# Optimization experiments

Hardware: AMD Instinct MI355X
Metric: run time of the kernel (lower is better)

## Reference

```python
import jax, jax.numpy as jnp
import numpy as np

B, T, D = 32, 2048, 80
K1 = K2 = 3
S1 = S2 = 2
CB_DIM, CB_SIZE = 512, 1024
MASK_P = 0.1
NOISE_STD = 0.1
INPUT_DIM = D * K1 * K2  # 720


def _win_idx(T_in, k, s):
    Tp = (T_in - k) // s + 1
    return jnp.arange(Tp)[:, None] * s + jnp.arange(k)[None, :]  # (Tp, k)


def _unfold(x, k, s):
    # matches torch x.unfold(1, k, s).view(B, Tp, -1): out[b, t, f*k + j] = x[b, t*s + j, f]
    idx = _win_idx(x.shape[1], k, s)
    w = x[:, idx, :]                 # (B, Tp, k, F)
    w = jnp.swapaxes(w, 2, 3)        # (B, Tp, F, k)
    return w.reshape(w.shape[0], w.shape[1], -1)


def setup_inputs() -> dict:
    key = jax.random.key(0)
    k1, k2, k3, k4, k5 = jax.random.split(key, 5)
    raw_feats = jax.random.normal(k1, (B, T, D), jnp.float32)
    auged_feats = jax.random.normal(k2, (B, T, D), jnp.float32)
    length = jax.random.randint(k3, (B,), T // 2, T + 1)
    xav = (2.0 / (INPUT_DIM + CB_DIM)) ** 0.5  # xavier_normal std
    projector = jax.random.normal(k4, (INPUT_DIM, CB_DIM), jnp.float32) * xav
    codebook = jax.random.normal(k5, (CB_SIZE, CB_DIM), jnp.float32)
    return {"raw_feats": raw_feats, "auged_feats": auged_feats, "length": length,
            "projector": projector, "codebook": codebook}


def reference(raw_feats, auged_feats, length, projector, codebook):
    T1 = (T - K1) // S1 + 1
    T2 = (T1 - K2) // S2 + 1
    idx1 = _win_idx(T, K1, S1)                         # (T1, K1)
    idx2 = _win_idx(T1, K2, S2)                        # (T2, K2)
    frame_windows = idx1[idx2].reshape(T2, K1 * K2)    # (T2, 9) original frame idx per subsampled step
    label_lengths = ((length - K1) // S1 + 1 - K2) // S2 + 1  # (B,)

    # --- label path: two torch-style unfolds -> project -> nearest codebook entry ---
    stacked = _unfold(_unfold(raw_feats, K1, S1), K2, S2)     # (B, T2, 720)
    targets = jnp.matmul(stacked, projector)                  # (B, T2, 512)
    # squared-euclidean expansion; same argmin as ||t - c||
    dist = (jnp.sum(targets * targets, axis=-1, keepdims=True)
            - 2.0 * jnp.einsum('btd,cd->btc', targets, codebook)
            + jnp.sum(codebook * codebook, axis=-1))          # (B, T2, 1024)
    labels = jnp.argmin(dist, axis=-1) + 1                    # labels start from 1; 0 = ignore idx
    valid = jnp.arange(T2)[None, :] < label_lengths[:, None]  # (B, T2)
    labels = jnp.where(valid, labels, 0)[None]                # (num_codebooks=1, B, T2)

    # --- static (span length 1) random masking on valid subsampled steps ---
    mkey = jax.random.key(42)
    km, kn = jax.random.split(mkey)
    masked = (jax.random.uniform(km, (B, T2)) < MASK_P) & valid
    masked_dim = masked.astype(jnp.float32)                   # (B, T2)
    # scatter masked subsampled steps back onto original frame indices (union of windows)
    hits = jnp.zeros((B, T), jnp.float32).at[:, frame_windows].add(masked_dim[:, :, None])
    frame_mask = hits > 0                                     # (B, T)
    noise = NOISE_STD * jax.random.normal(kn, (B, T, D), auged_feats.dtype)
    masked_feats = jnp.where(frame_mask[:, :, None], noise, auged_feats)
    return masked_feats, labels, masked_dim
```

## Files before the change

### kernel.cpp

```cpp
#include <hip/hip_runtime.h>
#include <cstdint>

#define B_    32
#define T_    2048
#define D_    80
#define T2_   511
#define NROW  16352
#define GK    720
#define CBD   512
#define CBS   1024
#define HMASK 8176
#define HN    2621440
#define NP    16384
#define KB    23
#define GLDS  (259*81*4)

using bfrag = __attribute__((ext_vector_type(8))) short;
using f32x4 = __attribute__((ext_vector_type(4))) float;
using s8    = __attribute__((ext_vector_type(8))) short;

__device__ inline ushort f2bf(float f){
  uint32_t u = __float_as_uint(f);
  uint32_t r = (u + 0x7FFFu + ((u >> 16) & 1u)) >> 16;
  return (ushort)r;
}
__device__ inline float bf2f(ushort h){ return __uint_as_float(((uint32_t)h) << 16); }

#define GLL16(gsrc, ldst) __builtin_amdgcn_global_load_lds( \
    (__attribute__((address_space(1))) void*)(gsrc), \
    (__attribute__((address_space(3))) void*)(ldst), 16, 0, 0)

__host__ __device__ inline uint32_t rotl_(uint32_t v, int d){ return (v<<d)|(v>>(32-d)); }

__host__ __device__ inline void tf2x32(uint32_t k0, uint32_t k1, uint32_t& x0, uint32_t& x1){
  uint32_t ks2 = k0 ^ k1 ^ 0x1BD11BDAu;
  x0 += k0; x1 += k1;
  const int r0[4] = {13,15,26,6}, r1[4] = {17,29,16,24};
#pragma unroll
  for (int i=0;i<4;i++){ x0 += x1; x1 = rotl_(x1, r0[i]); x1 ^= x0; }
  x0 += k1; x1 += ks2 + 1u;
#pragma unroll
  for (int i=0;i<4;i++){ x0 += x1; x1 = rotl_(x1, r1[i]); x1 ^= x0; }
  x0 += ks2; x1 += k0 + 2u;
#pragma unroll
  for (int i=0;i<4;i++){ x0 += x1; x1 = rotl_(x1, r0[i]); x1 ^= x0; }
  x0 += k0; x1 += k1 + 3u;
#pragma unroll
  for (int i=0;i<4;i++){ x0 += x1; x1 = rotl_(x1, r1[i]); x1 ^= x0; }
  x0 += k1; x1 += ks2 + 4u;
#pragma unroll
  for (int i=0;i<4;i++){ x0 += x1; x1 = rotl_(x1, r0[i]); x1 ^= x0; }
  x0 += ks2; x1 += k0 + 5u;
}

__device__ inline float erfinv_f(float x){
  float w = -log1pf(-x*x);
  float p;
  if (w < 5.0f){
    w -= 2.5f;
    p = 2.81022636e-08f;
    p = fmaf(p, w, 3.43273939e-07f);
    p = fmaf(p, w, -3.5233877e-06f);
    p = fmaf(p, w, -4.39150654e-06f);
    p = fmaf(p, w, 0.00021858087f);
    p = fmaf(p, w, -0.00125372503f);
    p = fmaf(p, w, -0.00417768164f);
    p = fmaf(p, w, 0.246640727f);
    p = fmaf(p, w, 1.50140941f);
  } else {
    w = sqrtf(w) - 3.0f;
    p = -0.000200214257f;
    p = fmaf(p, w, 0.000100950558f);
    p = fmaf(p, w, 0.00134934322f);
    p = fmaf(p, w, -0.00367342844f);
    p = fmaf(p, w, 0.00573950773f);
    p = fmaf(p, w, -0.0076224613f);
    p = fmaf(p, w, 0.00943887047f);
    p = fmaf(p, w, 1.00167406f);
    p = fmaf(p, w, 2.83297682f);
  }
  return p * x;
}

__device__ inline int label_len(int L){ return (((L - 3) / 2) - 2) / 2 + 1; }

__global__ void cbnorm_k(const float* __restrict__ cb, ushort* __restrict__ W0, ushort* __restrict__ W1){
  int c = blockIdx.x, lane = threadIdx.x;
  double s = 0.0;
  for (int k = lane; k < CBD; k += 64){ float v = cb[c*CBD + k]; s += (double)v * (double)v; }
#pragma unroll
  for (int off = 32; off; off >>= 1) s += __shfl_down(s, off);
  float nf = (float)s;
  nf = __shfl(nf, 0);
  size_t base = ((size_t)(KB-1)*CBS + c)*32;
  int sw = ((c >> 1) & 3) << 3;
  if (lane == 16){
    float h = -0.5f * nf;
    ushort h0 = f2bf(h); ushort h1 = f2bf(h - bf2f(h0));
    W0[base + (16 ^ sw)] = h0; W1[base + (16 ^ sw)] = h1;
  } else if (lane > 16 && lane < 32){
    W0[base + (lane ^ sw)] = 0; W1[base + (lane ^ sw)] = 0;
  }
}

__global__ __launch_bounds__(256) void gather_k(const float* __restrict__ raw,
                                                ushort* __restrict__ S0, ushort* __restrict__ S1){
  extern __shared__ float lraw[];
  int b = blockIdx.x >> 3, ch = blockIdx.x & 7;
  int t20 = ch * 64;
  int nt2 = (T2_ - t20 < 64) ? (T2_ - t20) : 64;
  int r0 = 4 * t20;
  int rows = (T_ - r0 < 259) ? (T_ - r0) : 259;
  int tid = threadIdx.x;
  const float4* gsrc = (const float4*)(raw + ((size_t)b*T_ + r0)*D_);
  int nf4 = rows * 20;
  for (int q = tid; q < nf4; q += 256){
    float4 v = gsrc[q];
    int row = q / 20, c4 = (q - row*20) * 4;
    float* dst = &lraw[row*81 + c4];
    dst[0]=v.x; dst[1]=v.y; dst[2]=v.z; dst[3]=v.w;
  }
  __syncthreads();
  int nl = tid >> 2, g = tid & 3;
  if (nl >= nt2) return;
  int n = b*T2_ + t20 + nl;
  int gs = g ^ ((n >> 1) & 3);
  for (int kb = 0; kb < KB; ++kb){
    s8 o0, o1;
#pragma unroll
    for (int j = 0; j < 8; ++j){
      int k = kb*32 + g*8 + j;
      float v = 0.f;
      if (k < GK){
        int d = k / 9, rem = k - 9*d;
        int k1 = rem / 3, k2 = rem - 3*k1;
        v = lraw[(4*nl + 2*k2 + k1)*81 + d];
      } else if (k == GK) v = 1.f;
      ushort h0 = f2bf(v); ushort h1 = f2bf(v - bf2f(h0));
      o0[j] = (short)h0; o1[j] = (short)h1;
    }
    size_t off = ((size_t)kb*NP + n)*32 + gs*8;
    *(s8*)&S0[off] = o0;
    *(s8*)&S1[off] = o1;
  }
}

__global__ __launch_bounds__(256) void wgemm_k(const float* __restrict__ P, const float* __restrict__ cb,
                                               float* __restrict__ Wp){
  __shared__ float sP[16][68];
  __shared__ float sC[16][68];
  int r0 = blockIdx.y * 64, c0 = blockIdx.x * 64;
  int kz = blockIdx.z;
  int tid = threadIdx.x, tx = tid & 15, ty = tid >> 4;
  float acc[4][4] = {};
  for (int k0 = kz * 128; k0 < kz * 128 + 128; k0 += 16){
    __syncthreads();
    {
      int r = tid >> 2, kq = tid & 3;
      int rr = r0 + r;
      float4 v = {0.f,0.f,0.f,0.f};
      if (rr < GK) v = *(const float4*)&P[rr * CBD + k0 + kq * 4];
      sP[kq*4+0][r] = v.x; sP[kq*4+1][r] = v.y; sP[kq*4+2][r] = v.z; sP[kq*4+3][r] = v.w;
      float4 w = *(const float4*)&cb[(c0 + r) * CBD + k0 + kq * 4];
      sC[kq*4+0][r] = w.x; sC[kq*4+1][r] = w.y; sC[kq*4+2][r] = w.z; sC[kq*4+3][r] = w.w;
    }
    __syncthreads();
#pragma unroll
    for (int kk = 0; kk < 16; ++kk){
      float4 a = *(const float4*)&sP[kk][ty * 4];
      float4 b = *(const float4*)&sC[kk][tx * 4];
      float av[4] = {a.x,a.y,a.z,a.w}, bv[4] = {b.x,b.y,b.z,b.w};
#pragma unroll
      for (int i = 0; i < 4; ++i)
#pragma unroll
        for (int j = 0; j < 4; ++j) acc[i][j] = fmaf(av[i], bv[j], acc[i][j]);
    }
  }
#pragma unroll
  for (int i = 0; i < 4; ++i){
    int r = r0 + ty * 4 + i;
    if (r < GK){
      float4 o; o.x = acc[i][0]; o.y = acc[i][1]; o.z = acc[i][2]; o.w = acc[i][3];
      *(float4*)&Wp[((size_t)kz * GK + r) * CBS + c0 + tx * 4] = o;
    }
  }
}

__global__ void wreduce_k(const float* __restrict__ Wp, ushort* __restrict__ W0, ushort* __restrict__ W1){
  int idx = blockIdx.x * 256 + threadIdx.x;
  int r = idx >> 10, c = idx & (CBS - 1);
  float v = Wp[(size_t)r * CBS + c]
          + Wp[((size_t)GK + r) * CBS + c]
          + Wp[((size_t)2*GK + r) * CBS + c]
          + Wp[((size_t)3*GK + r) * CBS + c];
  ushort h0 = f2bf(v); ushort h1 = f2bf(v - bf2f(h0));
  size_t o = ((size_t)(r >> 5) * CBS + c) * 32 + ((r & 31) ^ (((c >> 1) & 3) << 3));
  W0[o] = h0; W1[o] = h1;
}

__global__ __launch_bounds__(512, 2) void score_k(const ushort* __restrict__ S0, const ushort* __restrict__ S1,
                                                  const ushort* __restrict__ W0, const ushort* __restrict__ W1,
                                                  float* __restrict__ pval, int* __restrict__ pidx){
  extern __shared__ ushort lds[];
  int tid = threadIdx.x;
  int lane = tid & 63, wid = tid >> 6;
  int wm = wid >> 2, wn = wid & 3;
  int g = lane >> 4, lr = lane & 15;
  int gsw = g ^ ((lr >> 1) & 3);

  int id = blockIdx.x;
  int xcd = id & 7, slot = id >> 3;
  int cidx = slot & 3, ridx = (xcd << 3) | (slot >> 2);
  int n0 = ridx * 256, c0 = cidx * 256;

  int p = wid >> 1, h = wid & 1;
  const ushort* src0;
  size_t kstride;
  if      (p == 0){ src0 = S0 + (size_t)n0*32; kstride = (size_t)NP*32; }
  else if (p == 1){ src0 = S1 + (size_t)n0*32; kstride = (size_t)NP*32; }
  else if (p == 2){ src0 = W0 + (size_t)c0*32; kstride = (size_t)CBS*32; }
  else            { src0 = W1 + (size_t)c0*32; kstride = (size_t)CBS*32; }
  src0 += h * 4096;
  int doff = p * 8192 + h * 4096;

  f32x4 acc[8][4] = {};

#pragma unroll
  for (int q = 0; q < 8; ++q) GLL16(src0 + q*512 + lane*8, lds + doff + q*512);

  int abase = (wm*128 + lr)*32 + gsw*8;
  int bbase = (wn*64  + lr)*32 + gsw*8;

  for (int kb = 0; kb < KB; ++kb){
    const ushort* cur = lds + (kb & 1) * 32768;
    ushort*       nxt = lds + ((kb & 1) ^ 1) * 32768;
    asm volatile("s_waitcnt vmcnt(0)" ::: "memory");
    __builtin_amdgcn_s_barrier();

    const ushort* A0 = cur;
    const ushort* A1 = cur + 8192;
    const ushort* B0 = cur + 16384;
    const ushort* B1 = cur + 24576;

    bfrag a[4], b0f[4], b1f[4];
#pragma unroll
    for (int mt = 0; mt < 4; ++mt) a[mt] = *(const bfrag*)&A0[abase + mt*512];
#pragma unroll
    for (int nt = 0; nt < 4; ++nt) b0f[nt] = *(const bfrag*)&B0[bbase + nt*512];
    if (kb + 1 < KB){
      const ushort* s = src0 + (size_t)(kb+1)*kstride;
#pragma unroll
      for (int q = 0; q < 8; ++q) GLL16(s + q*512 + lane*8, nxt + doff + q*512);
    }
    asm volatile("s_waitcnt lgkmcnt(0)" ::: "memory");
    __builtin_amdgcn_sched_barrier(0);
    __builtin_amdgcn_s_setprio(1);
#pragma unroll
    for (int mt = 0; mt < 4; ++mt)
#pragma unroll
      for (int nt = 0; nt < 4; ++nt)
        acc[mt][nt] = __builtin_amdgcn_mfma_f32_16x16x32_bf16(a[mt], b0f[nt], acc[mt][nt], 0,0,0);
    __builtin_amdgcn_s_setprio(0);
    __builtin_amdgcn_sched_barrier(0);
    __builtin_amdgcn_s_barrier();
#pragma unroll
    for (int nt = 0; nt < 4; ++nt) b1f[nt] = *(const bfrag*)&B1[bbase + nt*512];
    asm volatile("s_waitcnt lgkmcnt(0)" ::: "memory");
    __builtin_amdgcn_sched_barrier(0);
    __builtin_amdgcn_s_setprio(1);
#pragma unroll
    for (int mt = 0; mt < 4; ++mt)
#pragma unroll
      for (int nt = 0; nt < 4; ++nt)
        acc[mt][nt] = __builtin_amdgcn_mfma_f32_16x16x32_bf16(a[mt], b1f[nt], acc[mt][nt], 0,0,0);
    __builtin_amdgcn_s_setprio(0);
    __builtin_amdgcn_sched_barrier(0);
    __builtin_amdgcn_s_barrier();
#pragma unroll
    for (int mt = 0; mt < 4; ++mt) a[mt] = *(const bfrag*)&A0[abase + (mt+4)*512];
    asm volatile("s_waitcnt lgkmcnt(0)" ::: "memory");
    __builtin_amdgcn_sched_barrier(0);
    __builtin_amdgcn_s_setprio(1);
#pragma unroll
    for (int mt = 0; mt < 4; ++mt)
#pragma unroll
      for (int nt = 0; nt < 4; ++nt)
        acc[4+mt][nt] = __builtin_amdgcn_mfma_f32_16x16x32_bf16(a[mt], b0f[nt], acc[4+mt][nt], 0,0,0);
#pragma unroll
    for (int mt = 0; mt < 4; ++mt)
#pragma unroll
      for (int nt = 0; nt < 4; ++nt)
        acc[4+mt][nt] = __builtin_amdgcn_mfma_f32_16x16x32_bf16(a[mt], b1f[nt], acc[4+mt][nt], 0,0,0);
    __builtin_amdgcn_s_setprio(0);
    __builtin_amdgcn_sched_barrier(0);
    __builtin_amdgcn_s_barrier();
    bfrag a1f[8];
#pragma unroll
    for (int mt = 0; mt < 8; ++mt) a1f[mt] = *(const bfrag*)&A1[abase + mt*512];
    asm volatile("s_waitcnt lgkmcnt(0)" ::: "memory");
    __builtin_amdgcn_sched_barrier(0);
    __builtin_amdgcn_s_setprio(1);
#pragma unroll
    for (int mt = 0; mt < 8; ++mt)
#pragma unroll
      for (int nt = 0; nt < 4; ++nt)
        acc[mt][nt] = __builtin_amdgcn_mfma_f32_16x16x32_bf16(a1f[mt], b0f[nt], acc[mt][nt], 0,0,0);
    __builtin_amdgcn_s_setprio(0);
    __builtin_amdgcn_sched_barrier(0);
  }

#pragma unroll
  for (int mt = 0; mt < 8; ++mt){
    float bv[4]; int bi[4];
#pragma unroll
    for (int r = 0; r < 4; ++r){
      float best = 3.4e38f; int besti = 0;
#pragma unroll
      for (int nt = 0; nt < 4; ++nt){
        float d = -2.f * acc[mt][nt][r];
        int c = c0 + wn*64 + nt*16 + lr;
        if (d < best){ best = d; besti = c; }
      }
      bv[r] = best; bi[r] = besti;
    }
#pragma unroll
    for (int off = 1; off < 16; off <<= 1){
#pragma unroll
      for (int r = 0; r < 4; ++r){
        float ov = __shfl_xor(bv[r], off);
        int   oi = __shfl_xor(bi[r], off);
        if (ov < bv[r] || (ov == bv[r] && oi < bi[r])){ bv[r] = ov; bi[r] = oi; }
      }
    }
    if (lr == 0){
      int pp = cidx*4 + wn;
#pragma unroll
      for (int r = 0; r < 4; ++r){
        int n = n0 + wm*128 + mt*16 + g*4 + r;
        pval[(size_t)pp*NP + n] = bv[r];
        pidx[(size_t)pp*NP + n] = bi[r];
      }
    }
  }
}

__device__ inline void emit_mask(const int* len, float* md, int i, uint32_t bits){
  float u = __uint_as_float((bits >> 9) | 0x3F800000u) - 1.0f;
  int b = i / T2_, t2 = i - b * T2_;
  bool m = (u < 0.1f) && (t2 < label_len(len[b]));
  md[i] = m ? 1.0f : 0.0f;
}

__device__ inline void comb_one(const float* __restrict__ pval, const int* __restrict__ pidx,
                                const int* __restrict__ len, float* __restrict__ lb, int n){
  float bv = pval[n]; int bi = pidx[n];
#pragma unroll
  for (int p = 1; p < 16; ++p){
    float v = pval[(size_t)p*NP + n]; int ii = pidx[(size_t)p*NP + n];
    if (v < bv || (v == bv && ii < bi)){ bv = v; bi = ii; }
  }
  int b = n / T2_, t2 = n - b * T2_;
  lb[n] = (t2 < label_len(len[b])) ? (float)(bi + 1) : 0.f;
}

__global__ void maskcomb_k(const float* __restrict__ pval, const int* __restrict__ pidx,
                           const int* __restrict__ len, float* __restrict__ lb,
                           float* __restrict__ md, uint32_t km0, uint32_t km1){
  int j = blockIdx.x * 256 + threadIdx.x;
  if (j >= HMASK) return;
  uint32_t x0 = (uint32_t)j, x1 = (uint32_t)(j + HMASK);
  tf2x32(km0, km1, x0, x1);
  emit_mask(len, md, j, x0);
  emit_mask(len, md, j + HMASK, x1);
  comb_one(pval, pidx, len, lb, j);
  comb_one(pval, pidx, len, lb, j + HMASK);
}

__device__ inline bool frame_masked(const float* md, int i){
  int tabs = i / D_;
  int t = tabs & (T_ - 1);
  int b = i / (D_ * T_);
  int lo = (t < 3) ? 0 : ((t - 3) >> 2);
  int hi = t >> 2; if (hi > T2_ - 1) hi = T2_ - 1;
  bool m = false;
  for (int t2 = lo; t2 <= hi; ++t2) m = m || (md[b * T2_ + t2] != 0.f);
  return m;
}

__device__ inline float noise_from_bits(uint32_t bits){
  float f = __uint_as_float((bits >> 9) | 0x3F800000u) - 1.0f;
  const float LOV = -0.99999994f;
  float u = fmaf(f, 2.0f, LOV);
  u = fmaxf(LOV, u);
  return 0.1f * (1.41421356f * erfinv_f(u));
}

__global__ void feats_k(const float* __restrict__ aug, const float* __restrict__ md,
                        float* __restrict__ mf, uint32_t kn0, uint32_t kn1){
  int j = blockIdx.x * 256 + threadIdx.x;
  bool m1 = frame_masked(md, j);
  bool m2 = frame_masked(md, j + HN);
  if (m1 || m2){
    uint32_t x0 = (uint32_t)j, x1 = (uint32_t)(j + HN);
    tf2x32(kn0, kn1, x0, x1);
    mf[j]      = m1 ? noise_from_bits(x0) : aug[j];
    mf[j + HN] = m2 ? noise_from_bits(x1) : aug[j + HN];
  } else {
    mf[j]      = aug[j];
    mf[j + HN] = aug[j + HN];
  }
}

extern "C" void kernel_launch(void* const* d_in, const int* in_sizes, int n_in,
                              void* d_out, int out_size, void* d_ws, size_t ws_size,
                              hipStream_t stream){
  const float* raw  = (const float*)d_in[0];
  const float* aug  = (const float*)d_in[1];
  const int*   len  = (const int*)  d_in[2];
  const float* proj = (const float*)d_in[3];
  const float* cb   = (const float*)d_in[4];

  float* out = (float*)d_out;
  float* mf  = out;
  float* lb  = out + 5242880;
  float* md  = out + 5259232;

  ushort* w  = (ushort*)d_ws;
  ushort* W0 = w;
  ushort* W1 = W0 + (size_t)KB*CBS*32;
  ushort* S0 = W1 + (size_t)KB*CBS*32;
  ushort* S1 = S0 + (size_t)KB*NP*32;
  float* pval = (float*)(S1 + (size_t)KB*NP*32);
  int*   pidx = (int*)(pval + (size_t)16*NP);
  float* Wp   = (float*)(pidx + (size_t)16*NP);

  hipFuncSetAttribute((const void*)score_k,  hipFuncAttributeMaxDynamicSharedMemorySize, 131072);
  hipFuncSetAttribute((const void*)gather_k, hipFuncAttributeMaxDynamicSharedMemorySize, GLDS);

  uint32_t a0 = 0u, a1 = 2u, b0 = 1u, b1 = 3u;
  tf2x32(0u, 42u, a0, a1);
  tf2x32(0u, 42u, b0, b1);
  uint32_t km0 = a0, km1 = b0, kn0 = a1, kn1 = b1;

  cbnorm_k<<<CBS, 64, 0, stream>>>(cb, W0, W1);
  wgemm_k<<<dim3(CBS / 64, 12, 4), 256, 0, stream>>>(proj, cb, Wp);
  wreduce_k<<<(GK * CBS) / 256, 256, 0, stream>>>(Wp, W0, W1);
  gather_k<<<256, 256, GLDS, stream>>>(raw, S0, S1);
  score_k<<<256, 512, 131072, stream>>>(S0, S1, W0, W1, pval, pidx);
  maskcomb_k<<<(HMASK + 255) / 256, 256, 0, stream>>>(pval, pidx, len, lb, md, km0, km1);
  feats_k<<<HN / 256, 256, 0, stream>>>(aug, md, mf, kn0, kn1);
}
```

Before: 147.8 us.

## Shrink score tiles to 128x128, fuse cbnorm into wreduce, vectorize feats

The score GEMM tile drops from 256x256 to 128x128 with 64KB LDS and four blocks per CU, giving 1024 blocks instead of 256. That doubles the partial argmin slices merged in the combine step to 32. The codebook-norm kernel is folded into wreduce as extra blocks to save a launch. The feats kernel now handles four elements per thread with float4 loads and stores and one mask check per row. Smaller tiles give better occupancy and load balance but reload more of each operand from memory.

```diff
diff --git a/kernel.cpp b/kernel.cpp
--- a/kernel.cpp
+++ b/kernel.cpp
@@ -84,25 +84,6 @@
 
 __device__ inline int label_len(int L){ return (((L - 3) / 2) - 2) / 2 + 1; }
 
-__global__ void cbnorm_k(const float* __restrict__ cb, ushort* __restrict__ W0, ushort* __restrict__ W1){
-  int c = blockIdx.x, lane = threadIdx.x;
-  double s = 0.0;
-  for (int k = lane; k < CBD; k += 64){ float v = cb[c*CBD + k]; s += (double)v * (double)v; }
-#pragma unroll
-  for (int off = 32; off; off >>= 1) s += __shfl_down(s, off);
-  float nf = (float)s;
-  nf = __shfl(nf, 0);
-  size_t base = ((size_t)(KB-1)*CBS + c)*32;
-  int sw = ((c >> 1) & 3) << 3;
-  if (lane == 16){
-    float h = -0.5f * nf;
-    ushort h0 = f2bf(h); ushort h1 = f2bf(h - bf2f(h0));
-    W0[base + (16 ^ sw)] = h0; W1[base + (16 ^ sw)] = h1;
-  } else if (lane > 16 && lane < 32){
-    W0[base + (lane ^ sw)] = 0; W1[base + (lane ^ sw)] = 0;
-  }
-}
-
 __global__ __launch_bounds__(256) void gather_k(const float* __restrict__ raw,
                                                 ushort* __restrict__ S0, ushort* __restrict__ S1){
   extern __shared__ float lraw[];
@@ -186,19 +167,41 @@
   }
 }
 
-__global__ void wreduce_k(const float* __restrict__ Wp, ushort* __restrict__ W0, ushort* __restrict__ W1){
-  int idx = blockIdx.x * 256 + threadIdx.x;
-  int r = idx >> 10, c = idx & (CBS - 1);
-  float v = Wp[(size_t)r * CBS + c]
-          + Wp[((size_t)GK + r) * CBS + c]
-          + Wp[((size_t)2*GK + r) * CBS + c]
-          + Wp[((size_t)3*GK + r) * CBS + c];
-  ushort h0 = f2bf(v); ushort h1 = f2bf(v - bf2f(h0));
-  size_t o = ((size_t)(r >> 5) * CBS + c) * 32 + ((r & 31) ^ (((c >> 1) & 3) << 3));
-  W0[o] = h0; W1[o] = h1;
-}
-
-__global__ __launch_bounds__(512, 2) void score_k(const ushort* __restrict__ S0, const ushort* __restrict__ S1,
+__global__ void wreduce_k(const float* __restrict__ Wp, const float* __restrict__ cb,
+                          ushort* __restrict__ W0, ushort* __restrict__ W1){
+  int bid = blockIdx.x;
+  if (bid < (GK * CBS) / 256){
+    int idx = bid * 256 + threadIdx.x;
+    int r = idx >> 10, c = idx & (CBS - 1);
+    float v = Wp[(size_t)r * CBS + c]
+            + Wp[((size_t)GK + r) * CBS + c]
+            + Wp[((size_t)2*GK + r) * CBS + c]
+            + Wp[((size_t)3*GK + r) * CBS + c];
+    ushort h0 = f2bf(v); ushort h1 = f2bf(v - bf2f(h0));
+    size_t o = ((size_t)(r >> 5) * CBS + c) * 32 + ((r & 31) ^ (((c >> 1) & 3) << 3));
+    W0[o] = h0; W1[o] = h1;
+  } else {
+    int c = (bid - (GK * CBS) / 256) * 4 + (threadIdx.x >> 6);
+    int lane = threadIdx.x & 63;
+    double s = 0.0;
+    for (int k = lane; k < CBD; k += 64){ float v = cb[c*CBD + k]; s += (double)v * (double)v; }
+#pragma unroll
+    for (int off = 32; off; off >>= 1) s += __shfl_down(s, off);
+    float nf = (float)s;
+    nf = __shfl(nf, 0);
+    size_t base = ((size_t)(KB-1)*CBS + c)*32;
+    int sw = ((c >> 1) & 3) << 3;
+    if (lane == 16){
+      float h = -0.5f * nf;
+      ushort h0 = f2bf(h); ushort h1 = f2bf(h - bf2f(h0));
+      W0[base + (16 ^ sw)] = h0; W1[base + (16 ^ sw)] = h1;
+    } else if (lane > 16 && lane < 32){
+      W0[base + (lane ^ sw)] = 0; W1[base + (lane ^ sw)] = 0;
+    }
+  }
+}
+
+__global__ __launch_bounds__(512, 4) void score_k(const ushort* __restrict__ S0, const ushort* __restrict__ S1,
                                                   const ushort* __restrict__ W0, const ushort* __restrict__ W1,
                                                   float* __restrict__ pval, int* __restrict__ pidx){
   extern __shared__ ushort lds[];
@@ -210,8 +213,8 @@
 
   int id = blockIdx.x;
   int xcd = id & 7, slot = id >> 3;
-  int cidx = slot & 3, ridx = (xcd << 3) | (slot >> 2);
-  int n0 = ridx * 256, c0 = cidx * 256;
+  int cidx = slot & 7, ridx = (xcd << 4) | (slot >> 3);
+  int n0 = ridx * 128, c0 = cidx * 128;
 
   int p = wid >> 1, h = wid & 1;
   const ushort* src0;
@@ -220,37 +223,40 @@
   else if (p == 1){ src0 = S1 + (size_t)n0*32; kstride = (size_t)NP*32; }
   else if (p == 2){ src0 = W0 + (size_t)c0*32; kstride = (size_t)CBS*32; }
   else            { src0 = W1 + (size_t)c0*32; kstride = (size_t)CBS*32; }
-  src0 += h * 4096;
-  int doff = p * 8192 + h * 4096;
-
-  f32x4 acc[8][4] = {};
-
-#pragma unroll
-  for (int q = 0; q < 8; ++q) GLL16(src0 + q*512 + lane*8, lds + doff + q*512);
-
-  int abase = (wm*128 + lr)*32 + gsw*8;
-  int bbase = (wn*64  + lr)*32 + gsw*8;
+  src0 += h * 2048;
+  int doff = p * 4096 + h * 2048;
+
+  f32x4 acc[4][2] = {};
+
+#pragma unroll
+  for (int q = 0; q < 4; ++q) GLL16(src0 + q*512 + lane*8, lds + doff + q*512);
+
+  int abase = (wm*64 + lr)*32 + gsw*8;
+  int bbase = (wn*32 + lr)*32 + gsw*8;
 
   for (int kb = 0; kb < KB; ++kb){
-    const ushort* cur = lds + (kb & 1) * 32768;
-    ushort*       nxt = lds + ((kb & 1) ^ 1) * 32768;
+    const ushort* cur = lds + (kb & 1) * 16384;
+    ushort*       nxt = lds + ((kb & 1) ^ 1) * 16384;
     asm volatile("s_waitcnt vmcnt(0)" ::: "memory");
     __builtin_amdgcn_s_barrier();
 
     const ushort* A0 = cur;
-    const ushort* A1 = cur + 8192;
-    const ushort* B0 = cur + 16384;
-    const ushort* B1 = cur + 24576;
-
-    bfrag a[4], b0f[4], b1f[4];
-#pragma unroll
-    for (int mt = 0; mt < 4; ++mt) a[mt] = *(const bfrag*)&A0[abase + mt*512];
-#pragma unroll
-    for (int nt = 0; nt < 4; ++nt) b0f[nt] = *(const bfrag*)&B0[bbase + nt*512];
+    const ushort* A1 = cur + 4096;
+    const ushort* B0 = cur + 8192;
+    const ushort* B1 = cur + 12288;
+
+    bfrag a0f[4], b0f[2], b1f[2];
+#pragma unroll
+    for (int mt = 0; mt < 4; ++mt) a0f[mt] = *(const bfrag*)&A0[abase + mt*512];
+#pragma unroll
+    for (int nt = 0; nt < 2; ++nt){
+      b0f[nt] = *(const bfrag*)&B0[bbase + nt*512];
+      b1f[nt] = *(const bfrag*)&B1[bbase + nt*512];
+    }
     if (kb + 1 < KB){
       const ushort* s = src0 + (size_t)(kb+1)*kstride;
 #pragma unroll
-      for (int q = 0; q < 8; ++q) GLL16(s + q*512 + lane*8, nxt + doff + q*512);
+      for (int q = 0; q < 4; ++q) GLL16(s + q*512 + lane*8, nxt + doff + q*512);
     }
     asm volatile("s_waitcnt lgkmcnt(0)" ::: "memory");
     __builtin_amdgcn_sched_barrier(0);
@@ -258,67 +264,40 @@
 #pragma unroll
     for (int mt = 0; mt < 4; ++mt)
 #pragma unroll
-      for (int nt = 0; nt < 4; ++nt)
-        acc[mt][nt] = __builtin_amdgcn_mfma_f32_16x16x32_bf16(a[mt], b0f[nt], acc[mt][nt], 0,0,0);
+      for (int nt = 0; nt < 2; ++nt)
+        acc[mt][nt] = __builtin_amdgcn_mfma_f32_16x16x32_bf16(a0f[mt], b0f[nt], acc[mt][nt], 0,0,0);
+#pragma unroll
+    for (int mt = 0; mt < 4; ++mt)
+#pragma unroll
+      for (int nt = 0; nt < 2; ++nt)
+        acc[mt][nt] = __builtin_amdgcn_mfma_f32_16x16x32_bf16(a0f[mt], b1f[nt], acc[mt][nt], 0,0,0);
     __builtin_amdgcn_s_setprio(0);
     __builtin_amdgcn_sched_barrier(0);
-    __builtin_amdgcn_s_barrier();
-#pragma unroll
-    for (int nt = 0; nt < 4; ++nt) b1f[nt] = *(const bfrag*)&B1[bbase + nt*512];
+    bfrag a1f[4];
+#pragma unroll
+    for (int mt = 0; mt < 4; ++mt) a1f[mt] = *(const bfrag*)&A1[abase + mt*512];
     asm volatile("s_waitcnt lgkmcnt(0)" ::: "memory");
     __builtin_amdgcn_sched_barrier(0);
     __builtin_amdgcn_s_setprio(1);
 #pragma unroll
     for (int mt = 0; mt < 4; ++mt)
 #pragma unroll
-      for (int nt = 0; nt < 4; ++nt)
-        acc[mt][nt] = __builtin_amdgcn_mfma_f32_16x16x32_bf16(a[mt], b1f[nt], acc[mt][nt], 0,0,0);
-    __builtin_amdgcn_s_setprio(0);
-    __builtin_amdgcn_sched_barrier(0);
-    __builtin_amdgcn_s_barrier();
-#pragma unroll
-    for (int mt = 0; mt < 4; ++mt) a[mt] = *(const bfrag*)&A0[abase + (mt+4)*512];
-    asm volatile("s_waitcnt lgkmcnt(0)" ::: "memory");
-    __builtin_amdgcn_sched_barrier(0);
-    __builtin_amdgcn_s_setprio(1);
-#pragma unroll
-    for (int mt = 0; mt < 4; ++mt)
-#pragma unroll
-      for (int nt = 0; nt < 4; ++nt)
-        acc[4+mt][nt] = __builtin_amdgcn_mfma_f32_16x16x32_bf16(a[mt], b0f[nt], acc[4+mt][nt], 0,0,0);
-#pragma unroll
-    for (int mt = 0; mt < 4; ++mt)
-#pragma unroll
-      for (int nt = 0; nt < 4; ++nt)
-        acc[4+mt][nt] = __builtin_amdgcn_mfma_f32_16x16x32_bf16(a[mt], b1f[nt], acc[4+mt][nt], 0,0,0);
-    __builtin_amdgcn_s_setprio(0);
-    __builtin_amdgcn_sched_barrier(0);
-    __builtin_amdgcn_s_barrier();
-    bfrag a1f[8];
-#pragma unroll
-    for (int mt = 0; mt < 8; ++mt) a1f[mt] = *(const bfrag*)&A1[abase + mt*512];
-    asm volatile("s_waitcnt lgkmcnt(0)" ::: "memory");
-    __builtin_amdgcn_sched_barrier(0);
-    __builtin_amdgcn_s_setprio(1);
-#pragma unroll
-    for (int mt = 0; mt < 8; ++mt)
-#pragma unroll
-      for (int nt = 0; nt < 4; ++nt)
+      for (int nt = 0; nt < 2; ++nt)
         acc[mt][nt] = __builtin_amdgcn_mfma_f32_16x16x32_bf16(a1f[mt], b0f[nt], acc[mt][nt], 0,0,0);
     __builtin_amdgcn_s_setprio(0);
     __builtin_amdgcn_sched_barrier(0);
   }
 
 #pragma unroll
-  for (int mt = 0; mt < 8; ++mt){
+  for (int mt = 0; mt < 4; ++mt){
     float bv[4]; int bi[4];
 #pragma unroll
     for (int r = 0; r < 4; ++r){
       float best = 3.4e38f; int besti = 0;
 #pragma unroll
-      for (int nt = 0; nt < 4; ++nt){
+      for (int nt = 0; nt < 2; ++nt){
         float d = -2.f * acc[mt][nt][r];
-        int c = c0 + wn*64 + nt*16 + lr;
+        int c = c0 + wn*32 + nt*16 + lr;
         if (d < best){ best = d; besti = c; }
       }
       bv[r] = best; bi[r] = besti;
@@ -336,7 +315,7 @@
       int pp = cidx*4 + wn;
 #pragma unroll
       for (int r = 0; r < 4; ++r){
-        int n = n0 + wm*128 + mt*16 + g*4 + r;
+        int n = n0 + wm*64 + mt*16 + g*4 + r;
         pval[(size_t)pp*NP + n] = bv[r];
         pidx[(size_t)pp*NP + n] = bi[r];
       }
@@ -355,7 +334,7 @@
                                 const int* __restrict__ len, float* __restrict__ lb, int n){
   float bv = pval[n]; int bi = pidx[n];
 #pragma unroll
-  for (int p = 1; p < 16; ++p){
+  for (int p = 1; p < 32; ++p){
     float v = pval[(size_t)p*NP + n]; int ii = pidx[(size_t)p*NP + n];
     if (v < bv || (v == bv && ii < bi)){ bv = v; bi = ii; }
   }
@@ -376,10 +355,7 @@
   comb_one(pval, pidx, len, lb, j + HMASK);
 }
 
-__device__ inline bool frame_masked(const float* md, int i){
-  int tabs = i / D_;
-  int t = tabs & (T_ - 1);
-  int b = i / (D_ * T_);
+__device__ inline bool frame_row_masked(const float* md, int b, int t){
   int lo = (t < 3) ? 0 : ((t - 3) >> 2);
   int hi = t >> 2; if (hi > T2_ - 1) hi = T2_ - 1;
   bool m = false;
@@ -397,18 +373,34 @@
 
 __global__ void feats_k(const float* __restrict__ aug, const float* __restrict__ md,
                         float* __restrict__ mf, uint32_t kn0, uint32_t kn1){
-  int j = blockIdx.x * 256 + threadIdx.x;
-  bool m1 = frame_masked(md, j);
-  bool m2 = frame_masked(md, j + HN);
-  if (m1 || m2){
-    uint32_t x0 = (uint32_t)j, x1 = (uint32_t)(j + HN);
-    tf2x32(kn0, kn1, x0, x1);
-    mf[j]      = m1 ? noise_from_bits(x0) : aug[j];
-    mf[j + HN] = m2 ? noise_from_bits(x1) : aug[j + HN];
-  } else {
-    mf[j]      = aug[j];
-    mf[j + HN] = aug[j + HN];
-  }
+  int q = blockIdx.x * 256 + threadIdx.x;
+  int e0 = q * 4;
+  int row1 = e0 / D_;
+  int t1 = row1 & (T_ - 1), b1 = row1 >> 11;
+  int e2 = e0 + HN;
+  int row2 = e2 / D_;
+  int t2 = row2 & (T_ - 1), b2 = row2 >> 11;
+  bool m1 = frame_row_masked(md, b1, t1);
+  bool m2 = frame_row_masked(md, b2, t2);
+  const float4* aug4 = (const float4*)aug;
+  float4* mf4 = (float4*)mf;
+  float4 o1 = aug4[q];
+  float4 o2 = aug4[q + HN/4];
+  if (m1 | m2){
+    uint32_t xs[4], ys[4];
+#pragma unroll
+    for (int i = 0; i < 4; ++i){
+      uint32_t x0 = (uint32_t)(e0 + i), x1 = (uint32_t)(e0 + i + HN);
+      tf2x32(kn0, kn1, x0, x1);
+      xs[i] = x0; ys[i] = x1;
+    }
+    if (m1){ o1.x = noise_from_bits(xs[0]); o1.y = noise_from_bits(xs[1]);
+             o1.z = noise_from_bits(xs[2]); o1.w = noise_from_bits(xs[3]); }
+    if (m2){ o2.x = noise_from_bits(ys[0]); o2.y = noise_from_bits(ys[1]);
+             o2.z = noise_from_bits(ys[2]); o2.w = noise_from_bits(ys[3]); }
+  }
+  mf4[q] = o1;
+  mf4[q + HN/4] = o2;
 }
 
 extern "C" void kernel_launch(void* const* d_in, const int* in_sizes, int n_in,
@@ -431,10 +423,10 @@
   ushort* S0 = W1 + (size_t)KB*CBS*32;
   ushort* S1 = S0 + (size_t)KB*NP*32;
   float* pval = (float*)(S1 + (size_t)KB*NP*32);
-  int*   pidx = (int*)(pval + (size_t)16*NP);
-  float* Wp   = (float*)(pidx + (size_t)16*NP);
-
-  hipFuncSetAttribute((const void*)score_k,  hipFuncAttributeMaxDynamicSharedMemorySize, 131072);
+  int*   pidx = (int*)(pval + (size_t)32*NP);
+  float* Wp   = (float*)(pidx + (size_t)32*NP);
+
+  hipFuncSetAttribute((const void*)score_k,  hipFuncAttributeMaxDynamicSharedMemorySize, 65536);
   hipFuncSetAttribute((const void*)gather_k, hipFuncAttributeMaxDynamicSharedMemorySize, GLDS);
 
   uint32_t a0 = 0u, a1 = 2u, b0 = 1u, b1 = 3u;
@@ -442,11 +434,10 @@
   tf2x32(0u, 42u, b0, b1);
   uint32_t km0 = a0, km1 = b0, kn0 = a1, kn1 = b1;
 
-  cbnorm_k<<<CBS, 64, 0, stream>>>(cb, W0, W1);
   wgemm_k<<<dim3(CBS / 64, 12, 4), 256, 0, stream>>>(proj, cb, Wp);
-  wreduce_k<<<(GK * CBS) / 256, 256, 0, stream>>>(Wp, W0, W1);
+  wreduce_k<<<(GK * CBS) / 256 + CBS / 4, 256, 0, stream>>>(Wp, cb, W0, W1);
   gather_k<<<256, 256, GLDS, stream>>>(raw, S0, S1);
-  score_k<<<256, 512, 131072, stream>>>(S0, S1, W0, W1, pval, pidx);
+  score_k<<<1024, 512, 65536, stream>>>(S0, S1, W0, W1, pval, pidx);
   maskcomb_k<<<(HMASK + 255) / 256, 256, 0, stream>>>(pval, pidx, len, lb, md, km0, km1);
-  feats_k<<<HN / 256, 256, 0, stream>>>(aug, md, mf, kn0, kn1);
-}
+  feats_k<<<HN / 4 / 256, 256, 0, stream>>>(aug, md, mf, kn0, kn1);
+}
```

Result: slower. 159.3 us (+7.7%).
